# Performance work log

Hardware: AMD Instinct MI355X
Metric: run time of the kernel (lower is better)

The kernel has to match this reference:

```python
import jax, jax.numpy as jnp
import numpy as np

N_NODES = 50000   # total nodes across all graphs in the batch
N_EDGES = 800000  # avg degree 16
F_IN = 64         # input_dim
HID = 128         # hidden_dim
N_GRAPHS = 500    # number of graphs (max batch id)
N_CLS = 10        # output_dim
MLP_HID = 50      # post_mp hidden width (hard-coded in module)


def setup_inputs() -> dict:
    key = jax.random.key(0)
    ks = jax.random.split(key, 11)
    x = jax.random.normal(ks[0], (N_NODES, F_IN), dtype=jnp.float32)
    edge_index = jax.random.randint(ks[1], (2, N_EDGES), 0, N_NODES, dtype=jnp.int64)
    batch = jnp.sort(jax.random.randint(ks[2], (N_NODES,), 0, N_GRAPHS, dtype=jnp.int64))
    # SAGEConv params (lin_l on aggregated neighbors, lin_r root weight)
    W_neigh = jax.random.normal(ks[3], (F_IN, HID), dtype=jnp.float32) / np.sqrt(F_IN)
    W_self = jax.random.normal(ks[4], (F_IN, HID), dtype=jnp.float32) / np.sqrt(F_IN)
    b = jax.random.normal(ks[5], (HID,), dtype=jnp.float32) * 0.01
    # post_mp: Linear(HID,50) -> ReLU -> Linear(50, N_CLS)
    W1 = jax.random.normal(ks[6], (HID, MLP_HID), dtype=jnp.float32) / np.sqrt(HID)
    b1 = jax.random.normal(ks[7], (MLP_HID,), dtype=jnp.float32) * 0.01
    W2 = jax.random.normal(ks[8], (MLP_HID, N_CLS), dtype=jnp.float32) / np.sqrt(MLP_HID)
    b2 = jax.random.normal(ks[9], (N_CLS,), dtype=jnp.float32) * 0.01
    return {"x": x, "edge_index": edge_index, "batch": batch,
            "W_neigh": W_neigh, "W_self": W_self, "b": b,
            "W1": W1, "b1": b1, "W2": W2, "b2": b2}


def reference(x, edge_index, batch, W_neigh, W_self, b, W1, b1, W2, b2):
    src, dst = edge_index[0], edge_index[1]
    # SAGEConv: mean-aggregate neighbor features, then linear + root weight
    agg = jax.ops.segment_sum(x[src], dst, num_segments=N_NODES)          # [N, F_IN]
    deg = jax.ops.segment_sum(jnp.ones((src.shape[0], 1), x.dtype), dst,
                              num_segments=N_NODES)                       # [N, 1]
    agg = agg / jnp.maximum(deg, 1.0)
    emb = agg @ W_neigh + x @ W_self + b                                  # [N, HID]
    h = jax.nn.relu(emb)
    # global mean pool over graphs
    pooled = jax.ops.segment_sum(h, batch, num_segments=N_GRAPHS)         # [G, HID]
    cnt = jax.ops.segment_sum(jnp.ones((h.shape[0], 1), h.dtype), batch,
                              num_segments=N_GRAPHS)                      # [G, 1]
    pooled = pooled / jnp.maximum(cnt, 1.0)
    # post_mp MLP + log_softmax
    logits = jax.nn.relu(pooled @ W1 + b1) @ W2 + b2                      # [G, N_CLS]
    return emb, jax.nn.log_softmax(logits, axis=1)
```

## Files before the change

kernel.cpp:

```cpp
#include <hip/hip_runtime.h>

#define N_NODES_C 50000
#define F_IN_C 64
#define HID_C 128
#define N_GRAPHS_C 500
#define N_CLS_C 10
#define MLP_HID_C 50
#define SCAN_TILE 1024
#define N_SCAN_BLK ((N_NODES_C + SCAN_TILE - 1) / SCAN_TILE)
#define N_TILES (N_NODES_C / 16)
#define N_RANGES 8
#define RANGE_SZ (N_NODES_C / N_RANGES)
#define S_STRIPES 64
#define ZROW N_NODES_C

using short8 = __attribute__((ext_vector_type(8))) short;
using f32x4  = __attribute__((ext_vector_type(4))) float;

__device__ __forceinline__ int bl_i(int v, int l) {
    return __builtin_amdgcn_readlane(v, l);
}
__device__ __forceinline__ float uf(unsigned u) { return __uint_as_float(u); }

__device__ __forceinline__ unsigned pk_bf16(float a, float b) {
    unsigned ua = __float_as_uint(a), ub = __float_as_uint(b);
    ua += 0x7FFFu + ((ua >> 16) & 1u);
    ub += 0x7FFFu + ((ub >> 16) & 1u);
    return (ua >> 16) | (ub & 0xFFFF0000u);
}

union U8 { unsigned u[4]; uint4 q; short8 s; };

__global__ __launch_bounds__(256) void prep_kernel(
    const float* __restrict__ x,
    const int* __restrict__ batch,
    unsigned* __restrict__ xh,
    int* __restrict__ start)
{
    int tid = blockIdx.x * 256 + threadIdx.x;
    int stride = gridDim.x * 256;
    const float2* xf2 = (const float2*)x;
    int nx = N_NODES_C * (F_IN_C / 2);
    int total = (N_NODES_C + 1) * (F_IN_C / 2);
    for (int i = tid; i < total; i += stride) {
        if (i < nx) { float2 v = xf2[i]; xh[i] = pk_bf16(v.x, v.y); }
        else        xh[i] = 0u;
    }
    for (int i = tid; i < N_NODES_C; i += stride) {
        int b = batch[i];
        if (i == 0) { for (int g = 0; g <= b; ++g) start[g] = 0; }
        else { int p = batch[i - 1]; for (int g = p + 1; g <= b; ++g) start[g] = i; }
        if (i == N_NODES_C - 1) { for (int g = b + 1; g <= N_GRAPHS_C; ++g) start[g] = N_NODES_C; }
    }
}

__global__ __launch_bounds__(1024) void hist2d_kernel(
    const int* __restrict__ dst, int* __restrict__ h, int n_edges, int stripe)
{
    __shared__ int lh[RANGE_SZ];
    int s = blockIdx.x >> 3, r = blockIdx.x & 7;
    int lo = r * RANGE_SZ;
    int t = threadIdx.x;
    for (int i = t; i < RANGE_SZ; i += 1024) lh[i] = 0;
    __syncthreads();
    int e1 = min(n_edges, (s + 1) * stripe);
    for (int e = s * stripe + t; e < e1; e += 1024) {
        int d = dst[e] - lo;
        if ((unsigned)d < (unsigned)RANGE_SZ) atomicAdd(&lh[d], 1);
    }
    __syncthreads();
    for (int i = t; i < RANGE_SZ; i += 1024)
        h[(size_t)s * N_NODES_C + lo + i] = lh[i];
}

__global__ __launch_bounds__(1024) void reduce_kernel(
    const int* __restrict__ h, int* __restrict__ p, int* __restrict__ deg_i,
    int* __restrict__ bsums)
{
    __shared__ int sred[1024];
    int t = threadIdx.x;
    int n = blockIdx.x * 1024 + t;
    int run = 0;
    if (n < N_NODES_C) {
        #pragma unroll 8
        for (int s = 0; s < S_STRIPES; ++s) {
            int c = h[(size_t)s * N_NODES_C + n];
            p[(size_t)s * N_NODES_C + n] = run;
            run += c;
        }
        deg_i[n] = run;
    }
    sred[t] = (n < N_NODES_C) ? run : 0;
    __syncthreads();
    for (int o = 512; o > 0; o >>= 1) {
        if (t < o) sred[t] += sred[t + o];
        __syncthreads();
    }
    if (t == 0) bsums[blockIdx.x] = sred[0];
}

__global__ __launch_bounds__(256) void scan3_kernel(
    const int* __restrict__ deg_i, const int* __restrict__ bsums,
    int* __restrict__ off, int n)
{
    __shared__ int s[256];
    __shared__ int sbp;
    int b = blockIdx.x;
    int t = threadIdx.x;
    if (t < 64) {
        int v = (t < b) ? bsums[t] : 0;
        #pragma unroll
        for (int m = 1; m < 64; m <<= 1) v += __shfl_xor(v, m, 64);
        if (t == 0) sbp = v;
    }
    int base = b * SCAN_TILE;
    int v4[4];
    int sum = 0;
    #pragma unroll
    for (int j = 0; j < 4; ++j) {
        int i = base + t * 4 + j;
        v4[j] = (i < n) ? deg_i[i] : 0;
        sum += v4[j];
    }
    s[t] = sum;
    __syncthreads();
    for (int o = 1; o < 256; o <<= 1) {
        int tmp = (t >= o) ? s[t - o] : 0;
        __syncthreads();
        s[t] += tmp;
        __syncthreads();
    }
    int run = s[t] - sum + sbp;
    #pragma unroll
    for (int j = 0; j < 4; ++j) {
        int i = base + t * 4 + j;
        if (i < n) off[i] = run;
        run += v4[j];
    }
    if (b == N_SCAN_BLK - 1 && t == 255) off[n] = sbp + s[255];
}

__global__ __launch_bounds__(1024) void scatter2d_kernel(
    const int* __restrict__ src, const int* __restrict__ dst,
    const int* __restrict__ off, const int* __restrict__ p,
    int* __restrict__ adj, int n_edges, int stripe)
{
    __shared__ int lcur[RANGE_SZ];
    int s = blockIdx.x >> 3, r = blockIdx.x & 7;
    int lo = r * RANGE_SZ;
    int t = threadIdx.x;
    for (int i = t; i < RANGE_SZ; i += 1024)
        lcur[i] = off[lo + i] + p[(size_t)s * N_NODES_C + lo + i];
    __syncthreads();
    int e1 = min(n_edges, (s + 1) * stripe);
    for (int e = s * stripe + t; e < e1; e += 1024) {
        int d = dst[e] - lo;
        if ((unsigned)d < (unsigned)RANGE_SZ) {
            int pos = atomicAdd(&lcur[d], 1);
            adj[pos] = src[e];
        }
    }
}

__global__ __launch_bounds__(256) void gather_mean_kernel(
    const unsigned* __restrict__ xh,
    const int* __restrict__ adj,
    const int* __restrict__ off,
    unsigned* __restrict__ agg)
{
    int t = threadIdx.x;
    int wave = t >> 6, lane = t & 63;
    int base = (blockIdx.x * 4 + wave) * 2;
    int n0 = base, n1 = base + 1;
    int o0 = off[n0], m0 = off[n0 + 1], e1v = off[n1 + 1];
    int d0 = m0 - o0;
    int o1 = m0, d1 = e1v - m0;
    int half = lane >> 5, col = lane & 31;
    float sx0 = 0.f, sy0 = 0.f, sx1 = 0.f, sy1 = 0.f;

    int dm = max(d0, d1);
    for (int j0 = 0; j0 < dm; j0 += 64) {
        int c0 = min(max(d0 - j0, 0), 64);
        int c1 = min(max(d1 - j0, 0), 64);
        int nid0 = (lane < c0) ? adj[o0 + j0 + lane] : ZROW;
        int nid1 = (lane < c1) ? adj[o1 + j0 + lane] : ZROW;
        int cm = max(c0, c1);
        for (int j = 0; j < cm; j += 16) {
            unsigned u[16];
            #pragma unroll
            for (int m = 0; m < 8; ++m) {
                int re = bl_i(nid0, j + 2 * m);
                int ro = bl_i(nid0, j + 2 * m + 1);
                int row = half ? ro : re;
                u[m] = xh[(size_t)row * 32 + col];
            }
            #pragma unroll
            for (int m = 0; m < 8; ++m) {
                int re = bl_i(nid1, j + 2 * m);
                int ro = bl_i(nid1, j + 2 * m + 1);
                int row = half ? ro : re;
                u[8 + m] = xh[(size_t)row * 32 + col];
            }
            #pragma unroll
            for (int m = 0; m < 8; ++m) {
                sx0 += uf(u[m] << 16); sy0 += uf(u[m] & 0xFFFF0000u);
            }
            #pragma unroll
            for (int m = 0; m < 8; ++m) {
                sx1 += uf(u[8 + m] << 16); sy1 += uf(u[8 + m] & 0xFFFF0000u);
            }
        }
    }
    sx0 += __shfl_xor(sx0, 32, 64); sy0 += __shfl_xor(sy0, 32, 64);
    sx1 += __shfl_xor(sx1, 32, 64); sy1 += __shfl_xor(sy1, 32, 64);
    if (half == 0) {
        float inv = 1.0f / fmaxf((float)d0, 1.0f);
        agg[(size_t)n0 * 32 + col] = pk_bf16(sx0 * inv, sy0 * inv);
    } else {
        float inv = 1.0f / fmaxf((float)d1, 1.0f);
        agg[(size_t)n1 * 32 + col] = pk_bf16(sx1 * inv, sy1 * inv);
    }
}

__global__ __launch_bounds__(256) void gemm_kernel(
    const unsigned* __restrict__ xh,
    const unsigned* __restrict__ agg,
    const float* __restrict__ Wn,
    const float* __restrict__ Ws,
    const float* __restrict__ bias,
    float* __restrict__ emb_out)
{
    __shared__ unsigned sWk[64 * 129];
    __shared__ float sb[128];
    int t = threadIdx.x;
    for (int e = t; e < 64 * 128; e += 256) {
        int kk = e >> 7, n = e & 127;
        float w0, w1;
        if (kk < 32) { w0 = Ws[(2 * kk) * 128 + n];      w1 = Ws[(2 * kk + 1) * 128 + n]; }
        else         { w0 = Wn[(2 * kk - 64) * 128 + n]; w1 = Wn[(2 * kk - 63) * 128 + n]; }
        sWk[kk * 129 + n] = pk_bf16(w0, w1);
    }
    if (t < 128) sb[t] = bias[t];
    __syncthreads();

    int wave = t >> 6, lane = t & 63;
    int lr = lane & 15, lg = lane >> 4;
    int tile = blockIdx.x * 4 + wave;
    if (tile >= N_TILES) return;

    const uint4* xr = (const uint4*)(xh + ((size_t)tile * 16 + lr) * 32);
    const uint4* ar = (const uint4*)(agg + ((size_t)tile * 16 + lr) * 32);
    U8 A[4];
    A[0].q = xr[lg];
    A[1].q = xr[4 + lg];
    A[2].q = ar[lg];
    A[3].q = ar[4 + lg];

    #pragma unroll
    for (int c = 0; c < 8; ++c) {
        float bv = sb[c * 16 + lr];
        f32x4 acc = {bv, bv, bv, bv};
        #pragma unroll
        for (int s = 0; s < 4; ++s) {
            U8 B;
            #pragma unroll
            for (int jj = 0; jj < 4; ++jj)
                B.u[jj] = sWk[(16 * s + 4 * lg + jj) * 129 + c * 16 + lr];
            acc = __builtin_amdgcn_mfma_f32_16x16x32_bf16(A[s].s, B.s, acc, 0, 0, 0);
        }
        #pragma unroll
        for (int r = 0; r < 4; ++r)
            emb_out[((size_t)tile * 16 + lg * 4 + r) * 128 + c * 16 + lr] = acc[r];
    }
}

__global__ __launch_bounds__(256) void poolhead_kernel(
    const float* __restrict__ emb, const int* __restrict__ start,
    const float* __restrict__ W1, const float* __restrict__ b1,
    const float* __restrict__ W2, const float* __restrict__ b2,
    float* __restrict__ logits_out)
{
    int g = blockIdx.x;
    int t = threadIdx.x;
    __shared__ float sp[HID_C];
    __shared__ float shid[MLP_HID_C];
    __shared__ float sl[N_CLS_C];
    __shared__ float4 red[256];

    int s0 = start[g], e0 = start[g + 1];
    int q = t & 31, r0 = t >> 5;
    const float4* e4 = (const float4*)emb;
    float4 acc = make_float4(0.f, 0.f, 0.f, 0.f);
    for (int r = s0 + r0; r < e0; r += 8) {
        float4 v = e4[(size_t)r * 32 + q];
        acc.x += fmaxf(v.x, 0.f); acc.y += fmaxf(v.y, 0.f);
        acc.z += fmaxf(v.z, 0.f); acc.w += fmaxf(v.w, 0.f);
    }
    red[t] = acc;
    __syncthreads();
    if (t < 32) {
        float4 a = red[t];
        #pragma unroll
        for (int r = 1; r < 8; ++r) {
            float4 b = red[t + 32 * r];
            a.x += b.x; a.y += b.y; a.z += b.z; a.w += b.w;
        }
        float inv = 1.0f / fmaxf((float)(e0 - s0), 1.0f);
        ((float4*)sp)[t] = make_float4(a.x * inv, a.y * inv, a.z * inv, a.w * inv);
    }
    __syncthreads();

    if (t < MLP_HID_C) {
        float a = b1[t];
        #pragma unroll 8
        for (int k = 0; k < HID_C; ++k) a += sp[k] * W1[k * MLP_HID_C + t];
        shid[t] = fmaxf(a, 0.0f);
    }
    __syncthreads();

    if (t < N_CLS_C) {
        float a = b2[t];
        #pragma unroll
        for (int k = 0; k < MLP_HID_C; ++k) a += shid[k] * W2[k * N_CLS_C + t];
        sl[t] = a;
    }
    __syncthreads();

    if (t < N_CLS_C) {
        float m = sl[0];
        #pragma unroll
        for (int i = 1; i < N_CLS_C; ++i) m = fmaxf(m, sl[i]);
        float sum = 0.0f;
        #pragma unroll
        for (int i = 0; i < N_CLS_C; ++i) sum += expf(sl[i] - m);
        logits_out[(size_t)g * N_CLS_C + t] = sl[t] - m - logf(sum);
    }
}

extern "C" void kernel_launch(void* const* d_in, const int* in_sizes, int n_in,
                              void* d_out, int out_size, void* d_ws, size_t ws_size,
                              hipStream_t stream) {
    const float* x      = (const float*)d_in[0];
    const int*   ei     = (const int*)d_in[1];
    const int*   batch  = (const int*)d_in[2];
    const float* Wn     = (const float*)d_in[3];
    const float* Ws     = (const float*)d_in[4];
    const float* bias   = (const float*)d_in[5];
    const float* W1     = (const float*)d_in[6];
    const float* b1     = (const float*)d_in[7];
    const float* W2     = (const float*)d_in[8];
    const float* b2     = (const float*)d_in[9];

    float* out = (float*)d_out;
    int n_edges = in_sizes[1] / 2;
    const int* src = ei;
    const int* dst = ei + n_edges;
    int stripe = (n_edges + S_STRIPES - 1) / S_STRIPES;

    int* deg_i   = (int*)d_ws;
    int* off     = deg_i + N_NODES_C;
    int* bsums   = off + (N_NODES_C + 1);
    int* start   = bsums + 64;
    unsigned* xh = (unsigned*)(start + (N_GRAPHS_C + 1) + 2);
    int* adj     = (int*)(xh + (size_t)(N_NODES_C + 1) * 32);
    unsigned* agg = (unsigned*)(adj + ((n_edges + 3) & ~3));
    int* h       = (int*)(agg + (size_t)N_NODES_C * 32);
    int* p       = h + (size_t)S_STRIPES * N_NODES_C;

    prep_kernel<<<1024, 256, 0, stream>>>(x, batch, xh, start);
    hist2d_kernel<<<S_STRIPES * N_RANGES, 1024, 0, stream>>>(dst, h, n_edges, stripe);
    reduce_kernel<<<N_SCAN_BLK, 1024, 0, stream>>>(h, p, deg_i, bsums);
    scan3_kernel<<<N_SCAN_BLK, 256, 0, stream>>>(deg_i, bsums, off, N_NODES_C);
    scatter2d_kernel<<<S_STRIPES * N_RANGES, 1024, 0, stream>>>(src, dst, off, p,
                                                                adj, n_edges, stripe);

    gather_mean_kernel<<<6250, 256, 0, stream>>>(xh, adj, off, agg);

    gemm_kernel<<<782, 256, 0, stream>>>(xh, agg, Wn, Ws, bias, out);

    poolhead_kernel<<<N_GRAPHS_C, 256, 0, stream>>>(out, start, W1, b1, W2, b2,
                                                    out + (size_t)N_NODES_C * HID_C);
}
```

Before: 94.75 us.

## Pad CSR adjacency to multiples of 32 and gather one node per wave

Each node's adjacency segment is padded to a multiple of 32 entries, and the padding is pre-filled with the zero-row index. The gather kernel can then drop per-lane bounds handling and process one node per wave in chunks of 32 neighbours, doubling the grid. The aim is to remove the load imbalance and masking overhead of pairing two nodes per wave. In exchange, every node with degree 16 now reads about 32 rows, half of them wasted zero-row loads (cached). The adjacency buffer also grows and must be filled every call.

After: 99.78 us. 1.05x slower.

```diff
diff --git a/kernel.cpp b/kernel.cpp
--- a/kernel.cpp
+++ b/kernel.cpp
@@ -13,6 +13,7 @@
 #define RANGE_SZ (N_NODES_C / N_RANGES)
 #define S_STRIPES 64
 #define ZROW N_NODES_C
+#define PAD_M 32
 
 using short8 = __attribute__((ext_vector_type(8))) short;
 using f32x4  = __attribute__((ext_vector_type(4))) float;
@@ -35,7 +36,9 @@
     const float* __restrict__ x,
     const int* __restrict__ batch,
     unsigned* __restrict__ xh,
-    int* __restrict__ start)
+    int* __restrict__ start,
+    int* __restrict__ adj,
+    int adj_cap)
 {
     int tid = blockIdx.x * 256 + threadIdx.x;
     int stride = gridDim.x * 256;
@@ -46,6 +49,7 @@
         if (i < nx) { float2 v = xf2[i]; xh[i] = pk_bf16(v.x, v.y); }
         else        xh[i] = 0u;
     }
+    for (int i = tid; i < adj_cap; i += stride) adj[i] = ZROW;
     for (int i = tid; i < N_NODES_C; i += stride) {
         int b = batch[i];
         if (i == 0) { for (int g = 0; g <= b; ++g) start[g] = 0; }
@@ -90,7 +94,7 @@
         }
         deg_i[n] = run;
     }
-    sred[t] = (n < N_NODES_C) ? run : 0;
+    sred[t] = (n < N_NODES_C) ? ((run + PAD_M - 1) & ~(PAD_M - 1)) : 0;
     __syncthreads();
     for (int o = 512; o > 0; o >>= 1) {
         if (t < o) sred[t] += sred[t + o];
@@ -119,7 +123,7 @@
     #pragma unroll
     for (int j = 0; j < 4; ++j) {
         int i = base + t * 4 + j;
-        v4[j] = (i < n) ? deg_i[i] : 0;
+        v4[j] = (i < n) ? ((deg_i[i] + PAD_M - 1) & ~(PAD_M - 1)) : 0;
         sum += v4[j];
     }
     s[t] = sum;
@@ -166,59 +170,41 @@
     const unsigned* __restrict__ xh,
     const int* __restrict__ adj,
     const int* __restrict__ off,
+    const int* __restrict__ deg_i,
     unsigned* __restrict__ agg)
 {
     int t = threadIdx.x;
     int wave = t >> 6, lane = t & 63;
-    int base = (blockIdx.x * 4 + wave) * 2;
-    int n0 = base, n1 = base + 1;
-    int o0 = off[n0], m0 = off[n0 + 1], e1v = off[n1 + 1];
-    int d0 = m0 - o0;
-    int o1 = m0, d1 = e1v - m0;
+    int node = blockIdx.x * 4 + wave;
+    int o = off[node];
+    int d = deg_i[node];
+    int dpad = (d + PAD_M - 1) & ~(PAD_M - 1);
     int half = lane >> 5, col = lane & 31;
-    float sx0 = 0.f, sy0 = 0.f, sx1 = 0.f, sy1 = 0.f;
-
-    int dm = max(d0, d1);
-    for (int j0 = 0; j0 < dm; j0 += 64) {
-        int c0 = min(max(d0 - j0, 0), 64);
-        int c1 = min(max(d1 - j0, 0), 64);
-        int nid0 = (lane < c0) ? adj[o0 + j0 + lane] : ZROW;
-        int nid1 = (lane < c1) ? adj[o1 + j0 + lane] : ZROW;
-        int cm = max(c0, c1);
-        for (int j = 0; j < cm; j += 16) {
+    float sx = 0.f, sy = 0.f;
+
+    for (int j0 = 0; j0 < dpad; j0 += 64) {
+        int c = min(dpad - j0, 64);
+        int nid = (lane < c) ? adj[o + j0 + lane] : ZROW;
+        for (int j = 0; j < c; j += 32) {
             unsigned u[16];
             #pragma unroll
-            for (int m = 0; m < 8; ++m) {
-                int re = bl_i(nid0, j + 2 * m);
-                int ro = bl_i(nid0, j + 2 * m + 1);
+            for (int m = 0; m < 16; ++m) {
+                int re = bl_i(nid, j + 2 * m);
+                int ro = bl_i(nid, j + 2 * m + 1);
                 int row = half ? ro : re;
                 u[m] = xh[(size_t)row * 32 + col];
             }
             #pragma unroll
-            for (int m = 0; m < 8; ++m) {
-                int re = bl_i(nid1, j + 2 * m);
-                int ro = bl_i(nid1, j + 2 * m + 1);
-                int row = half ? ro : re;
-                u[8 + m] = xh[(size_t)row * 32 + col];
+            for (int m = 0; m < 16; ++m) {
+                sx += uf(u[m] << 16); sy += uf(u[m] & 0xFFFF0000u);
             }
-            #pragma unroll
-            for (int m = 0; m < 8; ++m) {
-                sx0 += uf(u[m] << 16); sy0 += uf(u[m] & 0xFFFF0000u);
-            }
-            #pragma unroll
-            for (int m = 0; m < 8; ++m) {
-                sx1 += uf(u[8 + m] << 16); sy1 += uf(u[8 + m] & 0xFFFF0000u);
-            }
-        }
-    }
-    sx0 += __shfl_xor(sx0, 32, 64); sy0 += __shfl_xor(sy0, 32, 64);
-    sx1 += __shfl_xor(sx1, 32, 64); sy1 += __shfl_xor(sy1, 32, 64);
+        }
+    }
+    sx += __shfl_xor(sx, 32, 64);
+    sy += __shfl_xor(sy, 32, 64);
     if (half == 0) {
-        float inv = 1.0f / fmaxf((float)d0, 1.0f);
-        agg[(size_t)n0 * 32 + col] = pk_bf16(sx0 * inv, sy0 * inv);
-    } else {
-        float inv = 1.0f / fmaxf((float)d1, 1.0f);
-        agg[(size_t)n1 * 32 + col] = pk_bf16(sx1 * inv, sy1 * inv);
+        float inv = 1.0f / fmaxf((float)d, 1.0f);
+        agg[(size_t)node * 32 + col] = pk_bf16(sx * inv, sy * inv);
     }
 }
 
@@ -356,6 +342,7 @@
     const int* src = ei;
     const int* dst = ei + n_edges;
     int stripe = (n_edges + S_STRIPES - 1) / S_STRIPES;
+    int adj_cap = n_edges + (PAD_M - 1) * N_NODES_C;
 
     int* deg_i   = (int*)d_ws;
     int* off     = deg_i + N_NODES_C;
@@ -363,18 +350,18 @@
     int* start   = bsums + 64;
     unsigned* xh = (unsigned*)(start + (N_GRAPHS_C + 1) + 2);
     int* adj     = (int*)(xh + (size_t)(N_NODES_C + 1) * 32);
-    unsigned* agg = (unsigned*)(adj + ((n_edges + 3) & ~3));
+    unsigned* agg = (unsigned*)(adj + (((size_t)adj_cap + 3) & ~3ull));
     int* h       = (int*)(agg + (size_t)N_NODES_C * 32);
     int* p       = h + (size_t)S_STRIPES * N_NODES_C;
 
-    prep_kernel<<<1024, 256, 0, stream>>>(x, batch, xh, start);
+    prep_kernel<<<1024, 256, 0, stream>>>(x, batch, xh, start, adj, adj_cap);
     hist2d_kernel<<<S_STRIPES * N_RANGES, 1024, 0, stream>>>(dst, h, n_edges, stripe);
     reduce_kernel<<<N_SCAN_BLK, 1024, 0, stream>>>(h, p, deg_i, bsums);
     scan3_kernel<<<N_SCAN_BLK, 256, 0, stream>>>(deg_i, bsums, off, N_NODES_C);
     scatter2d_kernel<<<S_STRIPES * N_RANGES, 1024, 0, stream>>>(src, dst, off, p,
                                                                 adj, n_edges, stripe);
 
-    gather_mean_kernel<<<6250, 256, 0, stream>>>(xh, adj, off, agg);
+    gather_mean_kernel<<<12500, 256, 0, stream>>>(xh, adj, off, deg_i, agg);
 
     gemm_kernel<<<782, 256, 0, stream>>>(xh, agg, Wn, Ws, bias, out);
 
```
